# Performance work log

Measured on AMD Instinct MI355X. Metric: run time of the kernel, lower is better.

## Reference

```python
import jax, jax.numpy as jnp
import numpy as np
from jax import lax

BS, L, H = 8, 2048, 1024
NH, HD = 16, 64


def setup_inputs() -> dict:
    key = jax.random.key(0)
    ks = jax.random.split(key, 4)
    s = 1.0 / np.sqrt(H)
    xav = np.sqrt(2.0 / (NH + HD))  # xavier_normal_ for ReadingHead (fan_in=HD? torch uses dims (NH,HD))
    return {
        "hidden_states": jax.random.normal(ks[0], (BS, L, H), jnp.float32),
        "K1_w": jax.random.normal(ks[1], (H, NH * HD), jnp.float32) * s,
        "K1_b": jnp.zeros((NH * HD,), jnp.float32),
        "V1_w": jax.random.normal(ks[2], (H, NH * HD), jnp.float32) * s,
        "V1_b": jnp.zeros((NH * HD,), jnp.float32),
        "bidirection_weight": jnp.full((1, 1, NH, 1, 4), 0.25, jnp.float32),
        "ReadingHead": jax.random.normal(ks[3], (NH, HD), jnp.float32) * xav,
    }


def _nearest_valid_maps(valid, L):
    # valid: [bs, L, nh] bool. Returns fm, bm: [bs, L, 2, nh] int32, matching the
    # original sequential torch loop (including its use of len_index = L-1-j for the
    # backward map's slot 0).
    bs, _, nh = valid.shape
    mask_t = jnp.moveaxis(valid, 1, 0)  # [L, bs, nh]

    def step(carry, x):
        a, b = carry
        m, v = x
        nb = jnp.where(m, a, b)
        na = jnp.where(m, v, a)
        return (na, nb), (na, nb)

    zero = jnp.zeros((bs, nh), jnp.int32)
    idx_fwd = jnp.arange(1, L, dtype=jnp.int32)
    _, (fa, fb) = lax.scan(step, (zero, zero), (mask_t[1:], idx_fwd))
    fa = jnp.concatenate([zero[None], fa], axis=0)  # [L, bs, nh]
    fb = jnp.concatenate([zero[None], fb], axis=0)

    last = jnp.full((bs, nh), L - 1, jnp.int32)
    # backward loop stores len_index = L-1-j at position j when valid
    vals_bwd = (L - 1) - jnp.arange(L - 1, dtype=jnp.int32)
    _, (ba, bb) = lax.scan(step, (last, last), (mask_t[: L - 1], vals_bwd), reverse=True)
    ba = jnp.concatenate([ba, last[None]], axis=0)
    bb = jnp.concatenate([bb, last[None]], axis=0)

    fm = jnp.stack([fa, fb], axis=2).transpose(1, 0, 2, 3)  # [bs, L, 2, nh]
    bm = jnp.stack([ba, bb], axis=2).transpose(1, 0, 2, 3)
    return fm, bm


def reference(hidden_states, K1_w, K1_b, V1_w, V1_b, bidirection_weight, ReadingHead):
    bs, length, _ = hidden_states.shape
    nh, hd = ReadingHead.shape
    K1 = jax.nn.relu(hidden_states @ K1_w + K1_b).reshape(bs, length, nh, hd)
    V1 = jax.nn.relu(hidden_states @ V1_w + V1_b).reshape(bs, length, nh, hd)
    dots = jnp.einsum('blnh,nh->bln', K1, ReadingHead)
    valid = dots > 0.5
    fm, bm = _nearest_valid_maps(valid, length)
    # gather V along sequence dim with the two nearest-valid maps
    Vf = jnp.take_along_axis(V1, fm.reshape(bs, 2 * length, nh, 1), axis=1)
    Vf = Vf.reshape(bs, length, 2, nh, hd)
    Vb = jnp.take_along_axis(V1, bm.reshape(bs, 2 * length, nh, 1), axis=1)
    Vb = Vb.reshape(bs, length, 2, nh, hd)
    # [bs, L, 4, nh, hd] -> [bs, L, nh, hd, 4], weighted sum over the 4 registers
    new_states = jnp.concatenate([Vf, Vb], axis=2).transpose(0, 1, 3, 4, 2) * bidirection_weight
    context = new_states.sum(axis=-1).reshape(bs, length, nh * hd)
    return context
```

## Files before the change

### kernel.cpp

```cpp
#include <hip/hip_runtime.h>
#include <hip/hip_bf16.h>
#include <cstdint>

#define BS 8
#define SEQ 2048
#define HDIM 1024
#define NH 16
#define HD 64
#define M_ROWS (BS * SEQ)
#define N_COLS (2 * HDIM)
#define KDIM HDIM

#define DELTA 0.025f
#define PERH_CAP 2048

#define OFF_A      ((size_t)0)
#define OFF_BT     ((size_t)33554432)
#define OFF_FCNT   ((size_t)37748736)
#define OFF_FLIST  ((size_t)37748800)
#define OFF_BIAS   ((size_t)37879872)
#define OFF_CVH    ((size_t)41943040)
#define OFF_VALID  ((size_t)75497472)
#define OFF_MAPS   ((size_t)75759616)

typedef __attribute__((ext_vector_type(8))) __bf16 bf16x8;
typedef __attribute__((ext_vector_type(4))) float f32x4;
typedef __attribute__((ext_vector_type(8))) unsigned short ushort8;

__device__ __forceinline__ unsigned short f2bf(float f) {
    unsigned int x = __builtin_bit_cast(unsigned int, f);
    unsigned int r = x + 0x7fffu + ((x >> 16) & 1u);
    return (unsigned short)(r >> 16);
}
__device__ __forceinline__ float bf2f(unsigned short u) {
    return __builtin_bit_cast(float, (unsigned int)u << 16);
}

__device__ __forceinline__ void g2l16(const void* gp, void* lp) {
    __builtin_amdgcn_global_load_lds(
        (__attribute__((address_space(1))) void*)(void*)gp,
        (__attribute__((address_space(3))) void*)lp, 16, 0, 0);
}

__global__ __launch_bounds__(256) void prep_kernel(const float4* __restrict__ hs4,
                                                   unsigned short* __restrict__ Abf,
                                                   const float* __restrict__ K1w,
                                                   const float* __restrict__ V1w,
                                                   unsigned short* __restrict__ Bt,
                                                   const float* __restrict__ K1b,
                                                   const float* __restrict__ V1b,
                                                   float* __restrict__ bias,
                                                   int* __restrict__ fcnt) {
    __shared__ float tile[32][33];
    const int blk = blockIdx.x;
    const int t = threadIdx.x;
    if (blk < 8192) {
        int i = blk * 256 + t;
        float4 v0 = hs4[i * 2];
        float4 v1 = hs4[i * 2 + 1];
        uint4 o;
        o.x = (unsigned)f2bf(v0.x) | ((unsigned)f2bf(v0.y) << 16);
        o.y = (unsigned)f2bf(v0.z) | ((unsigned)f2bf(v0.w) << 16);
        o.z = (unsigned)f2bf(v1.x) | ((unsigned)f2bf(v1.y) << 16);
        o.w = (unsigned)f2bf(v1.z) | ((unsigned)f2bf(v1.w) << 16);
        ((uint4*)Abf)[i] = o;
    } else if (blk < 10240) {
        int lb = blk - 8192;
        int z = lb >> 10;
        int tk = (lb >> 5) & 31;
        int tn = lb & 31;
        const float* W = z ? V1w : K1w;
        int r = t >> 3;
        int c4 = (t & 7) * 4;
        const float4 v = *(const float4*)&W[(size_t)(tk * 32 + r) * 1024 + tn * 32 + c4];
        tile[r][c4 + 0] = v.x; tile[r][c4 + 1] = v.y;
        tile[r][c4 + 2] = v.z; tile[r][c4 + 3] = v.w;
        __syncthreads();
        int n = tn * 32 + r;
        int k = tk * 32 + c4;
        ushort4 o;
        o.x = f2bf(tile[c4 + 0][r]); o.y = f2bf(tile[c4 + 1][r]);
        o.z = f2bf(tile[c4 + 2][r]); o.w = f2bf(tile[c4 + 3][r]);
        *(ushort4*)&Bt[((size_t)z * 1024 + n) * 1024 + k] = o;
    } else {
        int i = (blk - 10240) * 256 + t;
        bias[i] = (i < 1024) ? K1b[i] : V1b[i - 1024];
        if (i < 16) fcnt[i] = 0;
    }
}

__global__ __launch_bounds__(256) void gemm_kernel(const unsigned short* __restrict__ Abf,
                                                   const unsigned short* __restrict__ Btbf,
                                                   const float* __restrict__ bias,
                                                   const float* __restrict__ RH,
                                                   unsigned short* __restrict__ CVh,
                                                   unsigned char* __restrict__ valid,
                                                   int* __restrict__ fcnt,
                                                   int* __restrict__ flist) {
    constexpr int K = KDIM, BK = 64;
    __shared__ unsigned short As[128 * BK];
    __shared__ unsigned short Bs[128 * BK];
    const int t = threadIdx.x;
    const int wave = t >> 6, lane = t & 63;
    const int wm = wave >> 1, wn = wave & 1;
    const int l16 = lane & 15, quad = lane >> 4;
    const int sw = l16 & 7;

    const int wgid = blockIdx.y * 16 + blockIdx.x;
    const int swz = (wgid & 7) * 256 + (wgid >> 3);
    const int m0 = (swz >> 4) * 128, n0 = (swz & 15) * 128;

    f32x4 zero4 = {0.f, 0.f, 0.f, 0.f};
    f32x4 acc[4][4];
#pragma unroll
    for (int i = 0; i < 4; i++)
#pragma unroll
        for (int j = 0; j < 4; j++) acc[i][j] = zero4;

    const int rr = t >> 3;
    const int gsw = (t ^ (t >> 3)) & 7;
    const unsigned short* gA = Abf + (size_t)(m0 + rr) * K + gsw * 8;
    const unsigned short* gB = Btbf + (size_t)(n0 + rr) * K + gsw * 8;
    char* lAs = (char*)As + (size_t)wave * 1024;
    char* lBs = (char*)Bs + (size_t)wave * 1024;

    for (int k0 = 0; k0 < K; k0 += BK) {
#pragma unroll
        for (int i = 0; i < 4; i++)
            g2l16(gA + (size_t)i * 32 * K + k0, lAs + i * 4096);
#pragma unroll
        for (int i = 0; i < 4; i++)
            g2l16(gB + (size_t)i * 32 * K + k0, lBs + i * 4096);
        __syncthreads();
#pragma unroll
        for (int h = 0; h < 2; h++) {
            bf16x8 af[4], bfr[4];
            const int hq = h * 4 + quad;
#pragma unroll
            for (int mt = 0; mt < 4; mt++)
                af[mt] = *(const bf16x8*)&As[(wm * 64 + mt * 16 + l16) * BK + (hq ^ sw) * 8];
#pragma unroll
            for (int nt = 0; nt < 4; nt++)
                bfr[nt] = *(const bf16x8*)&Bs[(wn * 64 + nt * 16 + l16) * BK + (hq ^ sw) * 8];
#pragma unroll
            for (int mt = 0; mt < 4; mt++)
#pragma unroll
                for (int nt = 0; nt < 4; nt++)
                    acc[mt][nt] = __builtin_amdgcn_mfma_f32_16x16x32_bf16(af[mt], bfr[nt], acc[mt][nt], 0, 0, 0);
        }
        __syncthreads();
    }
    if (n0 < HDIM) {
        const int n = (n0 >> 6) + wn;
        float rh[4], bv[4];
#pragma unroll
        for (int nt = 0; nt < 4; nt++) {
            int col = n * 64 + nt * 16 + l16;
            rh[nt] = RH[col];
            bv[nt] = bias[col];
        }
#pragma unroll
        for (int mt = 0; mt < 4; mt++) {
#pragma unroll
            for (int r = 0; r < 4; r++) {
                float p = 0.f;
#pragma unroll
                for (int nt = 0; nt < 4; nt++)
                    p += fmaxf(acc[mt][nt][r] + bv[nt], 0.f) * rh[nt];
#pragma unroll
                for (int s = 8; s >= 1; s >>= 1) p += __shfl_xor(p, s, 64);
                if (l16 == 0) {
                    int row = m0 + wm * 64 + mt * 16 + quad * 4 + r;
                    int b = row >> 11, l = row & (SEQ - 1);
                    valid[((size_t)b * NH + n) * SEQ + l] = (p > 0.5f) ? 1 : 0;
                    if (fabsf(p - 0.5f) < DELTA) {
                        int idx = atomicAdd(&fcnt[n], 1);
                        if (idx < PERH_CAP) flist[n * PERH_CAP + idx] = row;
                    }
                }
            }
        }
    } else {
        const int nv0 = n0 - HDIM;
#pragma unroll
        for (int mt = 0; mt < 4; mt++) {
            int gm = m0 + wm * 64 + mt * 16 + quad * 4;
#pragma unroll
            for (int nt = 0; nt < 4; nt++) {
                int gn = nv0 + wn * 64 + nt * 16 + l16;
                float bvv = bias[HDIM + gn];
#pragma unroll
                for (int r = 0; r < 4; r++)
                    CVh[(size_t)(gm + r) * HDIM + gn] = f2bf(fmaxf(acc[mt][nt][r] + bvv, 0.f));
            }
        }
    }
}

__global__ __launch_bounds__(512) void refine_kernel(const float* __restrict__ hs,
                                                     const float* __restrict__ K1w,
                                                     const float* __restrict__ K1b,
                                                     const float* __restrict__ RH,
                                                     const int* __restrict__ fcnt,
                                                     const int* __restrict__ flist,
                                                     unsigned char* __restrict__ valid) {
    __shared__ float Wl[128 * 64];
    const int n = blockIdx.x >> 5;
    const int g = blockIdx.x & 31;
    const int wave = threadIdx.x >> 6, d = threadIdx.x & 63;
    int cnt = fcnt[n];
    if (cnt > PERH_CAP) cnt = PERH_CAP;

    const int r0 = threadIdx.x >> 4;
    const int c4 = (threadIdx.x & 15) * 4;
    const float bn = K1b[n * 64 + d];
    const float rhn = RH[n * 64 + d];

    for (int base = g * 8; base < cnt; base += 32 * 8) {
        const int task = base + wave;
        const bool live = task < cnt;
        const int bl = live ? flist[n * PERH_CAP + task] : 0;
        const float* x = hs + (size_t)bl * HDIM;

        double acc0 = 0.0, acc1 = 0.0, acc2 = 0.0, acc3 = 0.0;
        for (int kc = 0; kc < KDIM; kc += 128) {
#pragma unroll
            for (int rr = 0; rr < 4; rr++) {
                const float4 v = *(const float4*)&K1w[(size_t)(kc + rr * 32 + r0) * 1024 + n * 64 + c4];
                *(float4*)&Wl[(rr * 32 + r0) * 64 + c4] = v;
            }
            __syncthreads();
            if (live) {
                for (int k = 0; k < 128; k += 32) {
                    float w[32];
#pragma unroll
                    for (int u = 0; u < 32; u++)
                        w[u] = Wl[(k + u) * 64 + d];
                    float4 xv[8];
#pragma unroll
                    for (int u = 0; u < 8; u++)
                        xv[u] = *(const float4*)(x + kc + k + u * 4);
#pragma unroll
                    for (int u = 0; u < 8; u++) {
                        acc0 += (double)xv[u].x * (double)w[u * 4 + 0];
                        acc1 += (double)xv[u].y * (double)w[u * 4 + 1];
                        acc2 += (double)xv[u].z * (double)w[u * 4 + 2];
                        acc3 += (double)xv[u].w * (double)w[u * 4 + 3];
                    }
                }
            }
            __syncthreads();
        }
        if (live) {
            double k1 = ((acc0 + acc1) + (acc2 + acc3)) + (double)bn;
            if (k1 < 0.0) k1 = 0.0;
            double contrib = k1 * (double)rhn;
#pragma unroll
            for (int s = 32; s >= 1; s >>= 1) contrib += __shfl_xor(contrib, s, 64);
            if (d == 0) {
                int b = bl >> 11, l = bl & (SEQ - 1);
                valid[((size_t)b * NH + n) * SEQ + l] = (contrib > 0.5) ? 1 : 0;
            }
        }
    }
}

__global__ __launch_bounds__(64) void scan_kernel(const unsigned char* __restrict__ valid,
                                                  ushort4* __restrict__ maps) {
    int bn = blockIdx.x;
    int lane = threadIdx.x;
    __shared__ unsigned int summ[64];

    const unsigned char* vp = valid + (size_t)bn * SEQ + lane * 32;
    uint4 c0 = *(const uint4*)vp;
    uint4 c1 = *(const uint4*)(vp + 16);
    unsigned int wds[8] = {c0.x, c0.y, c0.z, c0.w, c1.x, c1.y, c1.z, c1.w};
    unsigned int mask = 0;
#pragma unroll
    for (int i = 0; i < 8; i++) {
#pragma unroll
        for (int j = 0; j < 4; j++)
            mask |= (((wds[i] >> (8 * j)) & 0xffu) ? 1u : 0u) << (i * 4 + j);
    }

    int cnt = 0, va = 0, vb = 0;
#pragma unroll
    for (int tt = 0; tt < 32; tt++) {
        if (mask & (1u << tt)) { vb = va; va = lane * 32 + tt; cnt++; }
    }
    summ[lane] = (unsigned)((cnt > 2 ? 2 : cnt) | (va << 2) | (vb << 13));
    __syncthreads();
    int a = 0, bb_ = 0;
    for (int tt = 0; tt < lane; tt++) {
        unsigned s = summ[tt];
        int c = s & 3, sva = (s >> 2) & 2047, svb = (s >> 13) & 2047;
        if (c >= 2) { a = sva; bb_ = svb; }
        else if (c == 1) { bb_ = a; a = sva; }
    }
    unsigned int fres[32];
#pragma unroll
    for (int tt = 0; tt < 32; tt++) {
        if (mask & (1u << tt)) { bb_ = a; a = lane * 32 + tt; }
        fres[tt] = (unsigned)a | ((unsigned)bb_ << 16);
    }
    __syncthreads();

    unsigned int maskb = mask;
    if (lane == 63) maskb &= ~(1u << 31);
    cnt = 0; va = 0; vb = 0;
#pragma unroll
    for (int tt = 31; tt >= 0; tt--) {
        if (maskb & (1u << tt)) { vb = va; va = (SEQ - 1) - (lane * 32 + tt); cnt++; }
    }
    summ[lane] = (unsigned)((cnt > 2 ? 2 : cnt) | (va << 2) | (vb << 13));
    __syncthreads();
    int a2 = SEQ - 1, b2 = SEQ - 1;
    for (int tt = 63; tt > lane; tt--) {
        unsigned s = summ[tt];
        int c = s & 3, sva = (s >> 2) & 2047, svb = (s >> 13) & 2047;
        if (c >= 2) { a2 = sva; b2 = svb; }
        else if (c == 1) { b2 = a2; a2 = sva; }
    }
#pragma unroll
    for (int tt = 31; tt >= 0; tt--) {
        int j = lane * 32 + tt;
        if (maskb & (1u << tt)) { b2 = a2; a2 = (SEQ - 1) - j; }
        unsigned f = fres[tt];
        maps[(size_t)bn * SEQ + j] =
            make_ushort4((unsigned short)(f & 0xffffu), (unsigned short)(f >> 16),
                         (unsigned short)a2, (unsigned short)b2);
    }
}

__global__ __launch_bounds__(256) void gather_kernel(const unsigned short* __restrict__ CVh,
                                                     const ushort4* __restrict__ maps,
                                                     const float* __restrict__ bw,
                                                     float* __restrict__ out) {
    const int t = threadIdx.x;
    const int sub = t >> 7, tt = t & 127;
    const int n = tt >> 3, q8 = tt & 7;
    const int bl = blockIdx.x * 2 + sub;
    const int b = bl >> 11, l = bl & (SEQ - 1);
    const ushort4 m = maps[((size_t)(b * NH + n)) * SEQ + l];
    const float4 w = *(const float4*)&bw[n * 4];
    const size_t colbase = (size_t)(n * 64 + q8 * 8);
    const size_t rowb = (size_t)b * SEQ;
    const ushort8 u0 = *(const ushort8*)&CVh[(rowb + m.x) * HDIM + colbase];
    const ushort8 u1 = *(const ushort8*)&CVh[(rowb + m.y) * HDIM + colbase];
    const ushort8 u2 = *(const ushort8*)&CVh[(rowb + m.z) * HDIM + colbase];
    const ushort8 u3 = *(const ushort8*)&CVh[(rowb + m.w) * HDIM + colbase];
    float o[8];
#pragma unroll
    for (int e = 0; e < 8; e++)
        o[e] = w.x * bf2f(u0[e]) + w.y * bf2f(u1[e]) + w.z * bf2f(u2[e]) + w.w * bf2f(u3[e]);
    float* op = &out[(size_t)bl * (NH * HD) + n * 64 + q8 * 8];
    *(float4*)op       = make_float4(o[0], o[1], o[2], o[3]);
    *(float4*)(op + 4) = make_float4(o[4], o[5], o[6], o[7]);
}

extern "C" void kernel_launch(void* const* d_in, const int* in_sizes, int n_in,
                              void* d_out, int out_size, void* d_ws, size_t ws_size,
                              hipStream_t stream) {
    (void)in_sizes; (void)n_in; (void)out_size; (void)ws_size;
    const float* hs  = (const float*)d_in[0];
    const float* K1w = (const float*)d_in[1];
    const float* K1b = (const float*)d_in[2];
    const float* V1w = (const float*)d_in[3];
    const float* V1b = (const float*)d_in[4];
    const float* bw  = (const float*)d_in[5];
    const float* RH  = (const float*)d_in[6];
    float* out = (float*)d_out;
    char* ws = (char*)d_ws;

    unsigned short* Abf  = (unsigned short*)(ws + OFF_A);
    unsigned short* Btbf = (unsigned short*)(ws + OFF_BT);
    int* fcnt = (int*)(ws + OFF_FCNT);
    int* flist = (int*)(ws + OFF_FLIST);
    float* bias  = (float*)(ws + OFF_BIAS);
    unsigned short* CVh = (unsigned short*)(ws + OFF_CVH);
    unsigned char* valid = (unsigned char*)(ws + OFF_VALID);
    ushort4* maps = (ushort4*)(ws + OFF_MAPS);

    prep_kernel<<<10248, 256, 0, stream>>>((const float4*)hs, Abf,
                                           K1w, V1w, Btbf, K1b, V1b, bias, fcnt);
    gemm_kernel<<<dim3(N_COLS / 128, M_ROWS / 128), 256, 0, stream>>>(
        Abf, Btbf, bias, RH, CVh, valid, fcnt, flist);
    refine_kernel<<<NH * 32, 512, 0, stream>>>(
        hs, K1w, K1b, RH, fcnt, flist, valid);
    scan_kernel<<<BS * NH, 64, 0, stream>>>(valid, maps);
    gather_kernel<<<(BS * SEQ) / 2, 256, 0, stream>>>(CVh, maps, bw, out);
}
```

Before: 343.1 us.

## Register-tile refine kernel over four rows per wave, drop LDS weight staging

The refine kernel that recomputes borderline K1·ReadingHead dots in fp64 now has each wave process four flagged rows at once. Each weight element is loaded straight from global memory into registers and reused across those four rows, replacing the shared-memory tile and its block-wide barriers. Blocks shrink from 512 to 256 threads, and the accumulators drop from four to two per row. This cuts LDS traffic and synchronisation, at the cost of uncoalesced strided global weight loads, more register pressure, and a slightly different fp64 summation order.

Result: slower. 363.6 us (+6.0%).

```diff
diff --git a/kernel.cpp b/kernel.cpp
--- a/kernel.cpp
+++ b/kernel.cpp
@@ -197,67 +197,68 @@
     }
 }
 
-__global__ __launch_bounds__(512) void refine_kernel(const float* __restrict__ hs,
+#define RT 4
+__global__ __launch_bounds__(256) void refine_kernel(const float* __restrict__ hs,
                                                      const float* __restrict__ K1w,
                                                      const float* __restrict__ K1b,
                                                      const float* __restrict__ RH,
                                                      const int* __restrict__ fcnt,
                                                      const int* __restrict__ flist,
                                                      unsigned char* __restrict__ valid) {
-    __shared__ float Wl[128 * 64];
     const int n = blockIdx.x >> 5;
     const int g = blockIdx.x & 31;
     const int wave = threadIdx.x >> 6, d = threadIdx.x & 63;
     int cnt = fcnt[n];
     if (cnt > PERH_CAP) cnt = PERH_CAP;
-
-    const int r0 = threadIdx.x >> 4;
-    const int c4 = (threadIdx.x & 15) * 4;
+    const int wid = g * 4 + wave;
+
+    const float* wp = K1w + n * 64 + d;
     const float bn = K1b[n * 64 + d];
     const float rhn = RH[n * 64 + d];
 
-    for (int base = g * 8; base < cnt; base += 32 * 8) {
-        const int task = base + wave;
-        const bool live = task < cnt;
-        const int bl = live ? flist[n * PERH_CAP + task] : 0;
-        const float* x = hs + (size_t)bl * HDIM;
-
-        double acc0 = 0.0, acc1 = 0.0, acc2 = 0.0, acc3 = 0.0;
-        for (int kc = 0; kc < KDIM; kc += 128) {
-#pragma unroll
-            for (int rr = 0; rr < 4; rr++) {
-                const float4 v = *(const float4*)&K1w[(size_t)(kc + rr * 32 + r0) * 1024 + n * 64 + c4];
-                *(float4*)&Wl[(rr * 32 + r0) * 64 + c4] = v;
-            }
-            __syncthreads();
-            if (live) {
-                for (int k = 0; k < 128; k += 32) {
-                    float w[32];
-#pragma unroll
-                    for (int u = 0; u < 32; u++)
-                        w[u] = Wl[(k + u) * 64 + d];
-                    float4 xv[8];
-#pragma unroll
-                    for (int u = 0; u < 8; u++)
-                        xv[u] = *(const float4*)(x + kc + k + u * 4);
-#pragma unroll
-                    for (int u = 0; u < 8; u++) {
-                        acc0 += (double)xv[u].x * (double)w[u * 4 + 0];
-                        acc1 += (double)xv[u].y * (double)w[u * 4 + 1];
-                        acc2 += (double)xv[u].z * (double)w[u * 4 + 2];
-                        acc3 += (double)xv[u].w * (double)w[u * 4 + 3];
-                    }
+    for (int base = wid * RT; base < cnt; base += 128 * RT) {
+        bool live[RT];
+        const float* x[RT];
+#pragma unroll
+        for (int j = 0; j < RT; j++) {
+            live[j] = (base + j) < cnt;
+            const int bl = flist[n * PERH_CAP + (live[j] ? base + j : base)];
+            x[j] = hs + (size_t)bl * HDIM;
+        }
+        double a0[RT], a1[RT];
+#pragma unroll
+        for (int j = 0; j < RT; j++) { a0[j] = 0.0; a1[j] = 0.0; }
+
+        for (int k = 0; k < KDIM; k += 16) {
+            float w[16];
+#pragma unroll
+            for (int u = 0; u < 16; u++)
+                w[u] = wp[(size_t)(k + u) * 1024];
+#pragma unroll
+            for (int j = 0; j < RT; j++) {
+                float4 xv[4];
+#pragma unroll
+                for (int u = 0; u < 4; u++)
+                    xv[u] = *(const float4*)(x[j] + k + u * 4);
+#pragma unroll
+                for (int u = 0; u < 4; u++) {
+                    a0[j] += (double)xv[u].x * (double)w[u * 4 + 0];
+                    a1[j] += (double)xv[u].y * (double)w[u * 4 + 1];
+                    a0[j] += (double)xv[u].z * (double)w[u * 4 + 2];
+                    a1[j] += (double)xv[u].w * (double)w[u * 4 + 3];
                 }
             }
-            __syncthreads();
-        }
-        if (live) {
-            double k1 = ((acc0 + acc1) + (acc2 + acc3)) + (double)bn;
+        }
+#pragma unroll
+        for (int j = 0; j < RT; j++) {
+            if (!live[j]) continue;
+            double k1 = (a0[j] + a1[j]) + (double)bn;
             if (k1 < 0.0) k1 = 0.0;
             double contrib = k1 * (double)rhn;
 #pragma unroll
             for (int s = 32; s >= 1; s >>= 1) contrib += __shfl_xor(contrib, s, 64);
             if (d == 0) {
+                const int bl = flist[n * PERH_CAP + base + j];
                 int b = bl >> 11, l = bl & (SEQ - 1);
                 valid[((size_t)b * NH + n) * SEQ + l] = (contrib > 0.5) ? 1 : 0;
             }
@@ -385,7 +386,7 @@
                                            K1w, V1w, Btbf, K1b, V1b, bias, fcnt);
     gemm_kernel<<<dim3(N_COLS / 128, M_ROWS / 128), 256, 0, stream>>>(
         Abf, Btbf, bias, RH, CVh, valid, fcnt, flist);
-    refine_kernel<<<NH * 32, 512, 0, stream>>>(
+    refine_kernel<<<NH * 32, 256, 0, stream>>>(
         hs, K1w, K1b, RH, fcnt, flist, valid);
     scan_kernel<<<BS * NH, 64, 0, stream>>>(valid, maps);
     gather_kernel<<<(BS * SEQ) / 2, 256, 0, stream>>>(CVh, maps, bw, out);
```
